# Kernel tuning notes

Hardware: AMD Instinct MI355X
Metric: run time of the kernel (lower is better)

Reference implementation:

```python
import jax, jax.numpy as jnp
import numpy as np

VOCAB_SIZE = 8192
EMBED_DIM = 256


def setup_inputs() -> dict:
    key = jax.random.key(0)
    k1, k2 = jax.random.split(key)
    N = 16384  # batch(512) * num_slots(8) * tokens_per_slot(4)
    z = jax.random.normal(k1, (N, EMBED_DIM), dtype=jnp.float32)
    codebook = jax.random.normal(k2, (VOCAB_SIZE, EMBED_DIM), dtype=jnp.float32)
    return {"z": z, "codebook": codebook}


def reference(z, codebook):
    # Squared-distance cdist via the expansion ||z||^2 + ||e||^2 - 2 z.e^T
    z_sq = jnp.sum(z * z, axis=1, keepdims=True)            # [N, 1]
    e_sq = jnp.sum(codebook * codebook, axis=1)              # [V]
    dist = z_sq + e_sq - 2.0 * jnp.matmul(z, codebook.T)     # [N, V]
    tokens = jnp.argmin(dist, axis=-1)                       # [N] int
    z_q = codebook[tokens]                                   # [N, E] gather
    # one-hot reference count (side statistic in the original forward)
    ref_count = jnp.zeros((VOCAB_SIZE,), dtype=jnp.float32).at[tokens].add(1.0)
    return tokens, z_q, ref_count
```

## Files before the change

kernel.cpp:

```cpp
#include <hip/hip_runtime.h>
#include <math.h>

#define N_ROWS 16384
#define VOCAB  8192
#define EMB    256

#define BM 128
#define BV 128
#define BK 64
#define VSPLIT 8
#define VRANGE (VOCAB / VSPLIT)
#define NVT    (VRANGE / BV)
#define TAU 0.15f

typedef _Float16 half8 __attribute__((ext_vector_type(8)));
typedef _Float16 half4 __attribute__((ext_vector_type(4)));
typedef float floatx4 __attribute__((ext_vector_type(4)));

__device__ __forceinline__ void load_lds16(const _Float16* g, _Float16* l) {
    __builtin_amdgcn_global_load_lds(
        (const __attribute__((address_space(1))) void*)g,
        (__attribute__((address_space(3))) void*)l, 16, 0, 0);
}

__global__ void prep_kernel(const float* __restrict__ z, const float* __restrict__ cb,
                            _Float16* __restrict__ zh, _Float16* __restrict__ ch,
                            float* __restrict__ esq, float* __restrict__ cnt,
                            unsigned long long* __restrict__ rkey,
                            int* __restrict__ flagcnt) {
    const int b = blockIdx.x, t = threadIdx.x;
    if (b < VOCAB / 4) {
        const int row  = b * 4 + (t >> 6);
        const int lane = t & 63;
        const float4 f = *(const float4*)(cb + (size_t)row * EMB + lane * 4);
        half4 h;
        h.x = (_Float16)f.x; h.y = (_Float16)f.y; h.z = (_Float16)f.z; h.w = (_Float16)f.w;
        *(half4*)(ch + (size_t)row * EMB + lane * 4) = h;
        float s = f.x * f.x + f.y * f.y + f.z * f.z + f.w * f.w;
        #pragma unroll
        for (int off = 32; off > 0; off >>= 1) s += __shfl_down(s, off, 64);
        if (lane == 0) esq[row] = s;
        if (t < 4) cnt[b * 4 + t] = 0.0f;
        if (t >= 8 && t < 16) rkey[b * 8 + (t - 8)] = ~0ull;
        if (b == 0 && t == 4) flagcnt[0] = 0;
        if (b == 0 && t == 5) flagcnt[1] = 0;
    } else {
        const size_t idx4 = (size_t)(b - VOCAB / 4) * 256 + t;
        const float4 f = *(const float4*)(z + idx4 * 4);
        half4 h;
        h.x = (_Float16)f.x; h.y = (_Float16)f.y; h.z = (_Float16)f.z; h.w = (_Float16)f.w;
        *(half4*)(zh + idx4 * 4) = h;
    }
}

__global__ __launch_bounds__(256, 2)
void mfma_dist_kernel(const _Float16* __restrict__ zh, const _Float16* __restrict__ ch,
                      const float* __restrict__ esq,
                      float* __restrict__ pd1, float* __restrict__ pd2,
                      float* __restrict__ pd3,
                      int* __restrict__ pi1, int* __restrict__ pi2) {
    __shared__ _Float16 zs[BM * BK];
    __shared__ _Float16 cs[BV * BK];
    float* sc_d1 = (float*)zs;
    float* sc_d2 = sc_d1 + BM * 2;
    float* sc_d3 = sc_d2 + BM * 2;
    int*   sc_i1 = (int*)(sc_d3 + BM * 2);
    int*   sc_i2 = sc_i1 + BM * 2;

    const int row0  = blockIdx.x * BM;
    const int vbase = blockIdx.y * VRANGE;

    const int tid  = threadIdx.x;
    const int w    = tid >> 6;
    const int lane = tid & 63;
    const int lr   = lane & 15;
    const int quad = lane >> 4;
    const int mh   = (w >> 1) * 64;
    const int vh   = (w & 1) * 64;

    const int q7   = quad ^ (lr & 7);
    const int offA0 = q7 * 8;
    const int offA1 = (4 ^ q7) * 8;
    int rA[4], rB[4];
    #pragma unroll
    for (int i = 0; i < 4; ++i) { rA[i] = (mh + i * 16 + lr) * BK; rB[i] = (vh + i * 16 + lr) * BK; }

    const int schunk = (lane & 7) ^ (lane >> 3);
    const _Float16* zsrc = zh + (size_t)(row0 + w * 32 + (lane >> 3)) * EMB + schunk * 8;

    float m1[16], m2[16], m3[16]; int i1[16], i2[16];
    #pragma unroll
    for (int t = 0; t < 16; ++t) {
        m1[t] = -INFINITY; m2[t] = -INFINITY; m3[t] = -INFINITY; i1[t] = 0; i2[t] = 0;
    }

    float ev[4];
    #pragma unroll
    for (int j = 0; j < 4; ++j) ev[j] = esq[vbase + vh + j * 16 + lr];

    for (int vt = 0; vt < NVT; ++vt) {
        const int v0 = vbase + vt * BV;
        const _Float16* csrc = ch + (size_t)(v0 + w * 32 + (lane >> 3)) * EMB + schunk * 8;

        floatx4 acc[4][4];
        #pragma unroll
        for (int j = 0; j < 4; ++j) {
            const float e2 = -0.5f * ev[j];
            #pragma unroll
            for (int i = 0; i < 4; ++i) acc[i][j] = (floatx4)e2;
        }
        float evn[4];
        {
            const int vtn = (vt + 1 < NVT) ? vt + 1 : vt;
            #pragma unroll
            for (int j = 0; j < 4; ++j) evn[j] = esq[vbase + vtn * BV + vh + j * 16 + lr];
        }

        #pragma unroll 1
        for (int kt = 0; kt < EMB / BK; ++kt) {
            const int ko = kt * BK;
            #pragma unroll
            for (int q = 0; q < 4; ++q) {
                load_lds16(zsrc + (size_t)q * 8 * EMB + ko, &zs[w * 2048 + q * 512]);
                load_lds16(csrc + (size_t)q * 8 * EMB + ko, &cs[w * 2048 + q * 512]);
            }
            __syncthreads();

            #pragma unroll
            for (int s = 0; s < 2; ++s) {
                const int off = s ? offA1 : offA0;
                half8 a[4];
                #pragma unroll
                for (int i = 0; i < 4; ++i) a[i] = *(const half8*)&zs[rA[i] + off];
                #pragma unroll
                for (int j = 0; j < 4; ++j) {
                    const half8 b = *(const half8*)&cs[rB[j] + off];
                    #pragma unroll
                    for (int i = 0; i < 4; ++i)
                        acc[i][j] = __builtin_amdgcn_mfma_f32_16x16x32_f16(a[i], b, acc[i][j], 0, 0, 0);
                }
            }
            __syncthreads();
        }

        int vj[4];
        #pragma unroll
        for (int j = 0; j < 4; ++j) vj[j] = v0 + vh + j * 16 + lr;
        #pragma unroll
        for (int i = 0; i < 4; ++i) {
            #pragma unroll
            for (int reg = 0; reg < 4; ++reg) {
                const int t = i * 4 + reg;
                #pragma unroll
                for (int j = 0; j < 4; ++j) {
                    const float a = acc[i][j][reg];
                    const bool gt1 = a > m1[t];
                    const bool gt2 = a > m2[t];
                    const bool gt3 = a > m3[t];
                    m3[t] = gt2 ? m2[t] : (gt3 ? a : m3[t]);
                    m2[t] = gt1 ? m1[t] : (gt2 ? a : m2[t]);
                    i2[t] = gt1 ? i1[t] : (gt2 ? vj[j] : i2[t]);
                    m1[t] = gt1 ? a : m1[t];
                    i1[t] = gt1 ? vj[j] : i1[t];
                }
            }
        }
        #pragma unroll
        for (int j = 0; j < 4; ++j) ev[j] = evn[j];
    }

    #pragma unroll
    for (int t = 0; t < 16; ++t) {
        float a1 = m1[t], a2 = m2[t], a3 = m3[t]; int ii1 = i1[t], ii2 = i2[t];
        #pragma unroll
        for (int off = 1; off < 16; off <<= 1) {
            const float o1 = __shfl_xor(a1, off, 64);
            const float o2 = __shfl_xor(a2, off, 64);
            const float o3 = __shfl_xor(a3, off, 64);
            const int  oi1 = __shfl_xor(ii1, off, 64);
            const int  oi2 = __shfl_xor(ii2, off, 64);
            const bool g1 = o1 > a1, g2 = o1 > a2, g3 = o1 > a3;
            a3  = g2 ? a2  : (g3 ? o1  : a3);
            a2  = g1 ? a1  : (g2 ? o1  : a2);
            ii2 = g1 ? ii1 : (g2 ? oi1 : ii2);
            a1  = g1 ? o1  : a1;
            ii1 = g1 ? oi1 : ii1;
            const bool h2 = o2 > a2, h3 = o2 > a3;
            a3  = h2 ? a2  : (h3 ? o2 : a3);
            a2  = h2 ? o2  : a2;
            ii2 = h2 ? oi2 : ii2;
            a3 = fmaxf(a3, o3);
        }
        m1[t] = a1; m2[t] = a2; m3[t] = a3; i1[t] = ii1; i2[t] = ii2;
    }
    if (lr == 0) {
        #pragma unroll
        for (int t = 0; t < 16; ++t) {
            const int r = mh + (t >> 2) * 16 + quad * 4 + (t & 3);
            sc_d1[r * 2 + (w & 1)] = m1[t];
            sc_d2[r * 2 + (w & 1)] = m2[t];
            sc_d3[r * 2 + (w & 1)] = m3[t];
            sc_i1[r * 2 + (w & 1)] = i1[t];
            sc_i2[r * 2 + (w & 1)] = i2[t];
        }
    }
    __syncthreads();
    if (tid < BM) {
        float a1 = sc_d1[tid * 2], a2 = sc_d2[tid * 2], a3 = sc_d3[tid * 2];
        int  ii1 = sc_i1[tid * 2], ii2 = sc_i2[tid * 2];
        const float o1 = sc_d1[tid * 2 + 1], o2 = sc_d2[tid * 2 + 1], o3 = sc_d3[tid * 2 + 1];
        const int  oi1 = sc_i1[tid * 2 + 1], oi2 = sc_i2[tid * 2 + 1];
        {
            const bool g1 = o1 > a1, g2 = o1 > a2, g3 = o1 > a3;
            a3  = g2 ? a2  : (g3 ? o1  : a3);
            a2  = g1 ? a1  : (g2 ? o1  : a2);
            ii2 = g1 ? ii1 : (g2 ? oi1 : ii2);
            a1  = g1 ? o1  : a1;
            ii1 = g1 ? oi1 : ii1;
            const bool h2 = o2 > a2, h3 = o2 > a3;
            a3  = h2 ? a2  : (h3 ? o2 : a3);
            a2  = h2 ? o2  : a2;
            ii2 = h2 ? oi2 : ii2;
            a3 = fmaxf(a3, o3);
        }
        const size_t o = (size_t)blockIdx.y * N_ROWS + row0 + tid;
        pd1[o] = -2.0f * a1; pd2[o] = -2.0f * a2; pd3[o] = -2.0f * a3;
        pi1[o] = ii1; pi2[o] = ii2;
    }
}

__global__ void combine_kernel(const float* __restrict__ pd1, const float* __restrict__ pd2,
                               const float* __restrict__ pd3, const int* __restrict__ pi1,
                               const float* __restrict__ cb,
                               float* __restrict__ tokens, float* __restrict__ zq,
                               float* __restrict__ cnt,
                               int* __restrict__ flagcnt,
                               int* __restrict__ clist, int* __restrict__ flist) {
    const int wave = threadIdx.x >> 6;
    const int lane = threadIdx.x & 63;
    const int row  = blockIdx.x * 4 + wave;

    float g1 = INFINITY, g2 = INFINITY, mind3 = INFINITY; int gi = 0;
    #pragma unroll
    for (int s = 0; s < VSPLIT; ++s) {
        const size_t o = (size_t)s * N_ROWS + row;
        const float od1 = pd1[o], od2 = pd2[o], od3 = pd3[o]; const int oi1 = pi1[o];
        if (od1 < g1) { g2 = fminf(g1, od2); g1 = od1; gi = oi1; }
        else          { g2 = fminf(g2, od1); }
        mind3 = fminf(mind3, od3);
    }
    if ((g2 - g1) < TAU) {
        if (lane == 0) {
            if (mind3 >= g1 + TAU) {
                const int pos = atomicAdd(&flagcnt[0], 1);
                clist[pos] = row;
            } else {
                const int pos = atomicAdd(&flagcnt[1], 1);
                flist[pos] = row;
            }
        }
        return;
    }
    if (lane == 0) {
        tokens[row] = (float)gi;
        atomicAdd(&cnt[gi], 1.0f);
    }
    const float4 v = *(const float4*)(cb + (size_t)gi * EMB + lane * 4);
    *(float4*)(zq + (size_t)row * EMB + lane * 4) = v;
}

__global__ void rescue_cand_kernel(const int* __restrict__ flagcnt,
                                   const int* __restrict__ clist,
                                   const float* __restrict__ z, const float* __restrict__ cb,
                                   const float* __restrict__ esq,
                                   const int* __restrict__ pi1, const int* __restrict__ pi2,
                                   float* __restrict__ tokens, float* __restrict__ zq,
                                   float* __restrict__ cnt) {
    const int n    = flagcnt[0];
    const int w    = threadIdx.x >> 6;
    const int lane = threadIdx.x & 63;
    const int c    = lane >> 2;
    const int s    = lane & 3;

    for (int f = blockIdx.x * 4 + w; f < n; f += gridDim.x * 4) {
        const int row = clist[f];
        const size_t po = (size_t)(c & 7) * N_ROWS + row;
        const int cidx = (c < 8) ? pi1[po] : pi2[po];

        const float* zr = z  + (size_t)row  * EMB + s * 64;
        const float* cr = cb + (size_t)cidx * EMB + s * 64;
        float p0 = 0.0f, p1 = 0.0f, p2 = 0.0f, p3 = 0.0f;
        #pragma unroll
        for (int k = 0; k < 4; ++k) {
            const float4 z0 = *(const float4*)(zr + k * 16 + 0);
            const float4 c0 = *(const float4*)(cr + k * 16 + 0);
            const float4 z1 = *(const float4*)(zr + k * 16 + 4);
            const float4 c1 = *(const float4*)(cr + k * 16 + 4);
            const float4 z2 = *(const float4*)(zr + k * 16 + 8);
            const float4 c2 = *(const float4*)(cr + k * 16 + 8);
            const float4 z3 = *(const float4*)(zr + k * 16 + 12);
            const float4 c3 = *(const float4*)(cr + k * 16 + 12);
            p0 += z0.x * c0.x + z0.y * c0.y + z0.z * c0.z + z0.w * c0.w;
            p1 += z1.x * c1.x + z1.y * c1.y + z1.z * c1.z + z1.w * c1.w;
            p2 += z2.x * c2.x + z2.y * c2.y + z2.z * c2.z + z2.w * c2.w;
            p3 += z3.x * c3.x + z3.y * c3.y + z3.z * c3.z + z3.w * c3.w;
        }
        float p = (p0 + p1) + (p2 + p3);
        p += __shfl_xor(p, 1, 64);
        p += __shfl_xor(p, 2, 64);

        float bd = esq[cidx] - 2.0f * p;
        int   bv = cidx;
        #pragma unroll
        for (int off = 4; off < 64; off <<= 1) {
            const float od = __shfl_xor(bd, off, 64);
            const int   ov = __shfl_xor(bv, off, 64);
            if (od < bd || (od == bd && ov < bv)) { bd = od; bv = ov; }
        }
        if (lane == 0) {
            tokens[row] = (float)bv;
            atomicAdd(&cnt[bv], 1.0f);
        }
        const float4 c4 = *(const float4*)(cb + (size_t)bv * EMB + lane * 4);
        *(float4*)(zq + (size_t)row * EMB + lane * 4) = c4;
    }
}

#define RBV 64
#define RSPLIT 4
#define NTILE (VOCAB / RBV)
__global__ __launch_bounds__(256, 2)
void rescue_full_kernel(const int* __restrict__ flagcnt, const int* __restrict__ flist,
                        const float* __restrict__ z, const float* __restrict__ cb,
                        const float* __restrict__ esq,
                        unsigned long long* __restrict__ rkey) {
    const int n = __builtin_amdgcn_readfirstlane(flagcnt[1]);
    if (n == 0) return;

    __shared__ float cs[RBV][EMB];

    const int tile = blockIdx.x >> 2;
    const int rs   = blockIdx.x & 3;
    const int c0   = tile * RBV;
    const int tid  = threadIdx.x;
    const int w    = tid >> 6;
    const int lane = tid & 63;
    const int g    = lane >> 2;
    const int s    = lane & 3;

    #pragma unroll
    for (int i = 0; i < 16; ++i) {
        const int code = i * 4 + w;
        const float4 v = *(const float4*)(cb + (size_t)(c0 + code) * EMB + lane * 4);
        *(float4*)&cs[code][(lane ^ (code & 7)) * 4] = v;
    }
    __syncthreads();

    const int nq = (n + 3) >> 2;
    const int q0 = (rs << 2) | w;
    if (q0 >= nq) return;

    float ev[4];
    #pragma unroll
    for (int gs = 0; gs < 4; ++gs) ev[gs] = esq[c0 + gs * 16 + g];

    for (int q = q0; q < nq; q += 16) {
        int rows[4];
        #pragma unroll
        for (int r = 0; r < 4; ++r) {
            const int fi = q * 4 + r;
            rows[r] = __builtin_amdgcn_readfirstlane(flist[fi < n ? fi : 0]);
        }

        float p[4][4];
        #pragma unroll
        for (int gs = 0; gs < 4; ++gs)
            #pragma unroll
            for (int r = 0; r < 4; ++r) p[gs][r] = 0.0f;

        #pragma unroll
        for (int kb = 0; kb < 4; ++kb) {
            #pragma unroll
            for (int kk = 0; kk < 4; ++kk) {
                const int dbase = (kb * 4 + kk) * 16 + s * 4;
                float4 zv[4];
                #pragma unroll
                for (int r = 0; r < 4; ++r)
                    zv[r] = *(const float4*)(z + (size_t)rows[r] * EMB + dbase);
                const int dq = (kb * 4 + kk) * 4 + s;
                #pragma unroll
                for (int gs = 0; gs < 4; ++gs) {
                    const int code = gs * 16 + g;
                    const float4 c4 = *(const float4*)&cs[code][(dq ^ (code & 7)) * 4];
                    #pragma unroll
                    for (int r = 0; r < 4; ++r)
                        p[gs][r] += zv[r].x * c4.x + zv[r].y * c4.y
                                  + zv[r].z * c4.z + zv[r].w * c4.w;
                }
            }
        }

        #pragma unroll
        for (int gs = 0; gs < 4; ++gs)
            #pragma unroll
            for (int r = 0; r < 4; ++r) {
                float t = p[gs][r];
                t += __shfl_xor(t, 1, 64);
                t += __shfl_xor(t, 2, 64);
                p[gs][r] = t;
            }

        #pragma unroll
        for (int r = 0; r < 4; ++r) {
            float bd = INFINITY; int bv = 0;
            #pragma unroll
            for (int gs = 0; gs < 4; ++gs) {
                const float d = ev[gs] - 2.0f * p[gs][r];
                const int v = c0 + gs * 16 + g;
                if (d < bd) { bd = d; bv = v; }
            }
            #pragma unroll
            for (int off = 4; off < 64; off <<= 1) {
                const float od = __shfl_xor(bd, off, 64);
                const int   ov = __shfl_xor(bv, off, 64);
                if (od < bd || (od == bd && ov < bv)) { bd = od; bv = ov; }
            }
            if (lane == 0 && q * 4 + r < n) {
                unsigned int u = __float_as_uint(bd);
                u = (u & 0x80000000u) ? ~u : (u | 0x80000000u);
                atomicMin(rkey + rows[r], ((unsigned long long)u << 32) | (unsigned int)bv);
            }
        }
    }
}

__global__ void rescue_write_kernel(const int* __restrict__ flagcnt,
                                    const int* __restrict__ flist,
                                    const unsigned long long* __restrict__ rkey,
                                    const float* __restrict__ cb,
                                    float* __restrict__ tokens, float* __restrict__ zq,
                                    float* __restrict__ cnt) {
    const int w    = threadIdx.x >> 6;
    const int lane = threadIdx.x & 63;
    const int n = flagcnt[1];
    for (int f = blockIdx.x * 4 + w; f < n; f += gridDim.x * 4) {
        const int row = flist[f];
        const int v = (int)(unsigned int)(rkey[row] & 0xFFFFFFFFull);
        if (lane == 0) {
            tokens[row] = (float)v;
            atomicAdd(&cnt[v], 1.0f);
        }
        const float4 c4 = *(const float4*)(cb + (size_t)v * EMB + lane * 4);
        *(float4*)(zq + (size_t)row * EMB + lane * 4) = c4;
    }
}

__global__ void esq_kernel(const float* __restrict__ cb, float* __restrict__ esq) {
    const int wave = threadIdx.x >> 6;
    const int lane = threadIdx.x & 63;
    const int row  = blockIdx.x * 4 + wave;
    const float4 v = *(const float4*)(cb + (size_t)row * EMB + lane * 4);
    float s = v.x * v.x + v.y * v.y + v.z * v.z + v.w * v.w;
    #pragma unroll
    for (int off = 32; off > 0; off >>= 1) s += __shfl_down(s, off, 64);
    if (lane == 0) esq[row] = s;
}

#define FLSTR 36
__global__ __launch_bounds__(256, 2)
void fb_dist_kernel(const float* __restrict__ z, const float* __restrict__ cb,
                    const float* __restrict__ esq,
                    float* __restrict__ pdist, int* __restrict__ pidx) {
    __shared__ float zs[BM][FLSTR];
    __shared__ float es[BV][FLSTR];
    __shared__ float rdist[16][16];
    __shared__ int   ridx [16][16];
    const int row0 = blockIdx.x * BM, vbase = blockIdx.y * VRANGE;
    const int tid = threadIdx.x, wave = tid >> 6, lane = tid & 63;
    const int wly = (lane >> 3) & 7, wlx = lane & 7;
    const int wbase = (wave >> 1) * 64, cbase = (wave & 1) * 64;
    const int arow = wbase + wly, bcol = cbase + wlx;
    const int rowSlot = (wave >> 1) * 8 + wly, colSlot = (wave & 1) * 8 + wlx;
    const int sc4 = tid & 7, sr0 = tid >> 3;
    float best[8]; int bidx[8];
    #pragma unroll
    for (int i = 0; i < 8; ++i) { best[i] = INFINITY; bidx[i] = 0; }
    for (int vt = 0; vt < NVT; ++vt) {
        const int v0 = vbase + vt * BV;
        float acc[8][8];
        #pragma unroll
        for (int i = 0; i < 8; ++i)
            #pragma unroll
            for (int j = 0; j < 8; ++j) acc[i][j] = 0.0f;
        #pragma unroll 1
        for (int kt = 0; kt < EMB / 32; ++kt) {
            #pragma unroll
            for (int t = 0; t < 4; ++t) {
                const int r = sr0 + 32 * t;
                *(float4*)&zs[r][sc4 * 4] = *(const float4*)(z  + (size_t)(row0 + r) * EMB + kt * 32 + sc4 * 4);
                *(float4*)&es[r][sc4 * 4] = *(const float4*)(cb + (size_t)(v0 + r) * EMB + kt * 32 + sc4 * 4);
            }
            __syncthreads();
            #pragma unroll 1
            for (int k0 = 0; k0 < 8; ++k0) {
                const int kk = k0 * 4;
                float a[8][4];
                #pragma unroll
                for (int i = 0; i < 8; ++i) {
                    const float4 a4 = *(const float4*)&zs[arow + 8 * i][kk];
                    a[i][0] = a4.x; a[i][1] = a4.y; a[i][2] = a4.z; a[i][3] = a4.w;
                }
                #pragma unroll
                for (int j = 0; j < 8; ++j) {
                    const float4 b4 = *(const float4*)&es[bcol + 8 * j][kk];
                    #pragma unroll
                    for (int i = 0; i < 8; ++i) {
                        acc[i][j] += a[i][0] * b4.x; acc[i][j] += a[i][1] * b4.y;
                        acc[i][j] += a[i][2] * b4.z; acc[i][j] += a[i][3] * b4.w;
                    }
                }
            }
            __syncthreads();
        }
        #pragma unroll
        for (int j = 0; j < 8; ++j) {
            const int v = v0 + bcol + 8 * j;
            const float evv = esq[v];
            #pragma unroll
            for (int i = 0; i < 8; ++i) {
                const float d = evv - 2.0f * acc[i][j];
                if (d < best[i]) { best[i] = d; bidx[i] = v; }
            }
        }
    }
    for (int i = 0; i < 8; ++i) {
        rdist[rowSlot][colSlot] = best[i];
        ridx [rowSlot][colSlot] = bidx[i];
        __syncthreads();
        if (colSlot == 0) {
            float bd = rdist[rowSlot][0]; int bi = ridx[rowSlot][0];
            #pragma unroll
            for (int t = 1; t < 16; ++t) {
                const float d = rdist[rowSlot][t]; const int ii = ridx[rowSlot][t];
                if (d < bd || (d == bd && ii < bi)) { bd = d; bi = ii; }
            }
            const int row = row0 + wbase + 8 * i + wly;
            pdist[(size_t)blockIdx.y * N_ROWS + row] = bd;
            pidx [(size_t)blockIdx.y * N_ROWS + row] = bi;
        }
        __syncthreads();
    }
}

__global__ void fb_combine_kernel(const float* __restrict__ pdist, const int* __restrict__ pidx,
                                  const float* __restrict__ cb,
                                  float* __restrict__ tokens, float* __restrict__ zq,
                                  float* __restrict__ cnt) {
    const int wave = threadIdx.x >> 6, lane = threadIdx.x & 63;
    const int row = blockIdx.x * 4 + wave;
    float bd = INFINITY; int bi = 0;
    #pragma unroll
    for (int s = 0; s < VSPLIT; ++s) {
        const float d = pdist[(size_t)s * N_ROWS + row];
        const int ii  = pidx [(size_t)s * N_ROWS + row];
        if (d < bd || (d == bd && ii < bi)) { bd = d; bi = ii; }
    }
    if (lane == 0) { tokens[row] = (float)bi; atomicAdd(&cnt[bi], 1.0f); }
    const float4 v = *(const float4*)(cb + (size_t)bi * EMB + lane * 4);
    *(float4*)(zq + (size_t)row * EMB + lane * 4) = v;
}

extern "C" void kernel_launch(void* const* d_in, const int* in_sizes, int n_in,
                              void* d_out, int out_size, void* d_ws, size_t ws_size,
                              hipStream_t stream) {
    const float* z  = (const float*)d_in[0];
    const float* cb = (const float*)d_in[1];

    float* out    = (float*)d_out;
    float* tokens = out;
    float* zq     = out + N_ROWS;
    float* cnt    = out + N_ROWS + (size_t)N_ROWS * EMB;

    const size_t ZE = (size_t)N_ROWS * EMB, CE = (size_t)VOCAB * EMB, P = (size_t)VSPLIT * N_ROWS;
    const size_t NEED = (ZE + CE) * sizeof(_Float16) + VOCAB * 4
                      + 5 * P * 4 + (size_t)N_ROWS * 8 + 256 + 2 * (size_t)N_ROWS * 4;

    if (ws_size >= NEED) {
        char* p = (char*)d_ws;
        _Float16* zh = (_Float16*)p;            p += ZE * 2;
        _Float16* ch = (_Float16*)p;            p += CE * 2;
        float* esq   = (float*)p;               p += VOCAB * 4;
        float* pd1   = (float*)p;               p += P * 4;
        float* pd2   = (float*)p;               p += P * 4;
        float* pd3   = (float*)p;               p += P * 4;
        int*   pi1   = (int*)p;                 p += P * 4;
        int*   pi2   = (int*)p;                 p += P * 4;
        unsigned long long* rkey = (unsigned long long*)p;  p += (size_t)N_ROWS * 8;
        int*   flagcnt = (int*)p;               p += 256;
        int*   clist = (int*)p;                 p += (size_t)N_ROWS * 4;
        int*   flist = (int*)p;

        prep_kernel<<<VOCAB / 4 + (int)(ZE / 4 / 256), 256, 0, stream>>>(
            z, cb, zh, ch, esq, cnt, rkey, flagcnt);
        mfma_dist_kernel<<<dim3(N_ROWS / BM, VSPLIT), 256, 0, stream>>>(
            zh, ch, esq, pd1, pd2, pd3, pi1, pi2);
        combine_kernel<<<N_ROWS / 4, 256, 0, stream>>>(
            pd1, pd2, pd3, pi1, cb, tokens, zq, cnt, flagcnt, clist, flist);
        rescue_cand_kernel<<<512, 256, 0, stream>>>(
            flagcnt, clist, z, cb, esq, pi1, pi2, tokens, zq, cnt);
        rescue_full_kernel<<<NTILE * RSPLIT, 256, 0, stream>>>(
            flagcnt, flist, z, cb, esq, rkey);
        rescue_write_kernel<<<32, 256, 0, stream>>>(
            flagcnt, flist, rkey, cb, tokens, zq, cnt);
    } else {
        float* esq   = (float*)d_ws;
        float* pdist = esq + VOCAB;
        int*   pidx  = (int*)(pdist + P);
        hipMemsetAsync(cnt, 0, VOCAB * sizeof(float), stream);
        esq_kernel<<<VOCAB / 4, 256, 0, stream>>>(cb, esq);
        fb_dist_kernel<<<dim3(N_ROWS / BM, VSPLIT), 256, 0, stream>>>(z, cb, esq, pdist, pidx);
        fb_combine_kernel<<<N_ROWS / 4, 256, 0, stream>>>(pdist, pidx, cb, tokens, zq, cnt);
    }
}
```

Before: 215.5 us.

## Double-buffer LDS tiles and prefetch next K-step with async global-to-LDS loads

Splits the z and codebook LDS tiles into two buffers and issues the global_load_lds for the next K step, including the first step of the next vocab tile, before computing on the current buffer. Uses explicit vmcnt waits and raw s_barrier in place of __syncthreads. The goal is to hide global memory latency behind the MFMA work. LDS use doubles, which may limit occupancy at two blocks per CU. The hand-written waitcnt and barrier ordering, and the reuse of zs as scratch after the loop, need care to stay correct.

```diff
diff --git a/kernel.cpp b/kernel.cpp
--- a/kernel.cpp
+++ b/kernel.cpp
@@ -53,14 +53,50 @@
     }
 }
 
+#define KSTEP(KT, RD, WR, LASTSTEP)                                            \
+    {                                                                          \
+        if (!(LASTSTEP)) {                                                     \
+            const _Float16* csn_ = ((KT) < 3) ? csrc : (csrc + (size_t)BV * EMB); \
+            const int kon_ = (((KT) + 1) & 3) * BK;                            \
+            _Pragma("unroll")                                                  \
+            for (int q = 0; q < 4; ++q) {                                      \
+                load_lds16(zsrc + (size_t)q * 8 * EMB + kon_,                  \
+                           &zs[WR][w * 2048 + q * 512]);                       \
+                load_lds16(csn_ + (size_t)q * 8 * EMB + kon_,                  \
+                           &cs[WR][w * 2048 + q * 512]);                       \
+            }                                                                  \
+            asm volatile("s_waitcnt vmcnt(8)" ::: "memory");                   \
+        } else {                                                               \
+            asm volatile("s_waitcnt vmcnt(0)" ::: "memory");                   \
+        }                                                                      \
+        __builtin_amdgcn_s_barrier();                                          \
+        _Pragma("unroll")                                                      \
+        for (int s_ = 0; s_ < 2; ++s_) {                                       \
+            const int off_ = s_ ? offA1 : offA0;                               \
+            half8 a_[4];                                                       \
+            _Pragma("unroll")                                                  \
+            for (int i_ = 0; i_ < 4; ++i_)                                     \
+                a_[i_] = *(const half8*)&zs[RD][rA[i_] + off_];                \
+            _Pragma("unroll")                                                  \
+            for (int j_ = 0; j_ < 4; ++j_) {                                   \
+                const half8 b_ = *(const half8*)&cs[RD][rB[j_] + off_];        \
+                _Pragma("unroll")                                              \
+                for (int i_ = 0; i_ < 4; ++i_)                                 \
+                    acc[i_][j_] = __builtin_amdgcn_mfma_f32_16x16x32_f16(      \
+                        a_[i_], b_, acc[i_][j_], 0, 0, 0);                     \
+            }                                                                  \
+        }                                                                      \
+        __builtin_amdgcn_s_barrier();                                          \
+    }
+
 __global__ __launch_bounds__(256, 2)
 void mfma_dist_kernel(const _Float16* __restrict__ zh, const _Float16* __restrict__ ch,
                       const float* __restrict__ esq,
                       float* __restrict__ pd1, float* __restrict__ pd2,
                       float* __restrict__ pd3,
                       int* __restrict__ pi1, int* __restrict__ pi2) {
-    __shared__ _Float16 zs[BM * BK];
-    __shared__ _Float16 cs[BV * BK];
+    __shared__ _Float16 zs[2][BM * BK];
+    __shared__ _Float16 cs[2][BV * BK];
     float* sc_d1 = (float*)zs;
     float* sc_d2 = sc_d1 + BM * 2;
     float* sc_d3 = sc_d2 + BM * 2;
@@ -98,6 +134,15 @@
     #pragma unroll
     for (int j = 0; j < 4; ++j) ev[j] = esq[vbase + vh + j * 16 + lr];
 
+    {
+        const _Float16* csrc0 = ch + (size_t)(vbase + w * 32 + (lane >> 3)) * EMB + schunk * 8;
+        #pragma unroll
+        for (int q = 0; q < 4; ++q) {
+            load_lds16(zsrc  + (size_t)q * 8 * EMB, &zs[0][w * 2048 + q * 512]);
+            load_lds16(csrc0 + (size_t)q * 8 * EMB, &cs[0][w * 2048 + q * 512]);
+        }
+    }
+
     for (int vt = 0; vt < NVT; ++vt) {
         const int v0 = vbase + vt * BV;
         const _Float16* csrc = ch + (size_t)(v0 + w * 32 + (lane >> 3)) * EMB + schunk * 8;
@@ -116,32 +161,10 @@
             for (int j = 0; j < 4; ++j) evn[j] = esq[vbase + vtn * BV + vh + j * 16 + lr];
         }
 
-        #pragma unroll 1
-        for (int kt = 0; kt < EMB / BK; ++kt) {
-            const int ko = kt * BK;
-            #pragma unroll
-            for (int q = 0; q < 4; ++q) {
-                load_lds16(zsrc + (size_t)q * 8 * EMB + ko, &zs[w * 2048 + q * 512]);
-                load_lds16(csrc + (size_t)q * 8 * EMB + ko, &cs[w * 2048 + q * 512]);
-            }
-            __syncthreads();
-
-            #pragma unroll
-            for (int s = 0; s < 2; ++s) {
-                const int off = s ? offA1 : offA0;
-                half8 a[4];
-                #pragma unroll
-                for (int i = 0; i < 4; ++i) a[i] = *(const half8*)&zs[rA[i] + off];
-                #pragma unroll
-                for (int j = 0; j < 4; ++j) {
-                    const half8 b = *(const half8*)&cs[rB[j] + off];
-                    #pragma unroll
-                    for (int i = 0; i < 4; ++i)
-                        acc[i][j] = __builtin_amdgcn_mfma_f32_16x16x32_f16(a[i], b, acc[i][j], 0, 0, 0);
-                }
-            }
-            __syncthreads();
-        }
+        KSTEP(0, 0, 1, false)
+        KSTEP(1, 1, 0, false)
+        KSTEP(2, 0, 1, false)
+        KSTEP(3, 1, 0, (vt == NVT - 1))
 
         int vj[4];
         #pragma unroll
@@ -228,6 +251,7 @@
         pi1[o] = ii1; pi2[o] = ii2;
     }
 }
+#undef KSTEP
 
 __global__ void combine_kernel(const float* __restrict__ pd1, const float* __restrict__ pd2,
                                const float* __restrict__ pd3, const int* __restrict__ pi1,
```

Result: faster. 210.5 us (-2.3%).
